# Performance work log

Measured on AMD Instinct MI355X. Metric: run time of the kernel, lower is better.

The kernel has to match this reference:

```python
import jax, jax.numpy as jnp
import numpy as np

DIM = 2048
N_HEADS = 32
N_KV_HEADS = 8
HEAD_DIM = DIM // N_HEADS  # 64
N_REP = N_HEADS // N_KV_HEADS  # 4
ROPE_BASE = 10000.0


def _rope_cos_sin(seq_len, head_dim, dtype):
    inv_freq = 1.0 / (ROPE_BASE ** (jnp.arange(0, head_dim, 2, dtype=jnp.float32) / head_dim))
    freqs = jnp.arange(seq_len, dtype=jnp.float32)[:, None] * inv_freq[None, :]  # [S, hd/2]
    return jnp.cos(freqs).astype(dtype), jnp.sin(freqs).astype(dtype)


def _apply_rope(x, cos, sin):
    # x: [B, S, H, hd]; cos/sin: [S, hd/2]
    x1, x2 = jnp.split(x, 2, axis=-1)
    c = cos[None, :, None, :]
    s = sin[None, :, None, :]
    return jnp.concatenate([x1 * c - x2 * s, x1 * s + x2 * c], axis=-1)


def setup_inputs() -> dict:
    key = jax.random.key(0)
    ks = jax.random.split(key, 5)
    B, S = 2, 2048
    x = jax.random.normal(ks[0], (B, S, DIM), dtype=jnp.float32)
    scale = 1.0 / np.sqrt(DIM)
    wq = jax.random.normal(ks[1], (DIM, DIM), dtype=jnp.float32) * scale
    wk = jax.random.normal(ks[2], (N_KV_HEADS * HEAD_DIM, DIM), dtype=jnp.float32) * scale
    wv = jax.random.normal(ks[3], (N_KV_HEADS * HEAD_DIM, DIM), dtype=jnp.float32) * scale
    wo = jax.random.normal(ks[4], (DIM, DIM), dtype=jnp.float32) * scale
    return {"x": x, "wq": wq, "wk": wk, "wv": wv, "wo": wo}


def reference(x, wq, wk, wv, wo):
    B, S, D = x.shape
    # projections (nn.Linear: y = x @ W.T)
    xq = (x @ wq.T).reshape(B, S, N_HEADS, HEAD_DIM)
    xk = (x @ wk.T).reshape(B, S, N_KV_HEADS, HEAD_DIM)
    xv = (x @ wv.T).reshape(B, S, N_KV_HEADS, HEAD_DIM)

    cos, sin = _rope_cos_sin(S, HEAD_DIM, x.dtype)
    xq = _apply_rope(xq, cos, sin)
    xk = _apply_rope(xk, cos, sin)

    # GQA: repeat kv heads
    keys = jnp.repeat(xk, N_REP, axis=2)    # [B, S, H, hd]
    values = jnp.repeat(xv, N_REP, axis=2)

    scores = jnp.einsum('bqhd,bkhd->bhqk', xq, keys) / np.sqrt(HEAD_DIM)
    causal = jnp.tril(jnp.ones((S, S), dtype=bool))
    scores = jnp.where(causal[None, None, :, :], scores, jnp.finfo(scores.dtype).min)
    probs = jax.nn.softmax(scores, axis=-1)
    out = jnp.einsum('bhqk,bkhd->bqhd', probs, values).reshape(B, S, D)
    return out @ wo.T  # dropout in eval mode == identity
```

## Files before the change

kernel.cpp:

```cpp
#include <hip/hip_runtime.h>

typedef __attribute__((ext_vector_type(8))) short bf16x8;
typedef __attribute__((ext_vector_type(4))) float f32x4;
typedef __attribute__((ext_vector_type(4))) unsigned short u16x4;

#define GPTR(p) (const __attribute__((address_space(1))) void*)(p)
#define LPTR(p) (__attribute__((address_space(3))) void*)(p)

static __device__ __forceinline__ unsigned short f2bf(float f) {
  union { float f; unsigned int u; } x; x.f = f;
  unsigned int u = x.u;
  unsigned int r = (u + 0x7fffu + ((u >> 16) & 1u)) >> 16;
  return (unsigned short)r;
}
static __device__ __forceinline__ float bf2f(unsigned short h) {
  union { unsigned int u; float f; } x; x.u = ((unsigned int)h) << 16;
  return x.f;
}
static __device__ __forceinline__ f32x4 f32x4_zero() {
  f32x4 z = {0.f, 0.f, 0.f, 0.f}; return z;
}
static __device__ __forceinline__ unsigned int cvt_pk_bf16(float lo, float hi) {
  unsigned int r;
  asm("v_cvt_pk_bf16_f32 %0, %1, %2" : "=v"(r) : "v"(lo), "v"(hi));
  return r;
}

__global__ void rope_table_kernel(float* __restrict__ costab, float* __restrict__ sintab) {
  int i = blockIdx.x * blockDim.x + threadIdx.x;
  int s = i >> 5, d = i & 31;
  float invf = exp2f(-(float)d * (13.287712379549449f / 32.0f));
  float a = (float)s * invf;
  costab[i] = cosf(a);
  sintab[i] = sinf(a);
}

__global__ void f32_to_bf16(const float* __restrict__ src, unsigned short* __restrict__ dst, int n4) {
  int stride = gridDim.x * blockDim.x;
  for (int i = blockIdx.x * blockDim.x + threadIdx.x; i < n4; i += stride) {
    float4 v = ((const float4*)src)[i];
    u16x4 o;
    o.x = f2bf(v.x); o.y = f2bf(v.y); o.z = f2bf(v.z); o.w = f2bf(v.w);
    *(u16x4*)(dst + (size_t)i * 4) = o;
  }
}

template<int OUT_BF16>
__global__ __launch_bounds__(256) void gemm_bt(const unsigned short* __restrict__ A,
                                               const unsigned short* __restrict__ B,
                                               void* __restrict__ Cv, int N, int K) {
  __shared__ __align__(16) unsigned short lsA[128 * 32];
  __shared__ __align__(16) unsigned short lsB[128 * 32];
  const int tid = threadIdx.x;
  const int wave = tid >> 6, lane = tid & 63;
  const int fq = lane >> 4, fr = lane & 15;
  const int wr = wave >> 1, wc = wave & 1;
  const int m0 = blockIdx.y * 128, n0 = blockIdx.x * 128;

  const unsigned short* ga0 = A + (size_t)(m0 + (tid >> 2)) * K + ((tid & 3) << 3);
  const unsigned short* ga1 = ga0 + (size_t)64 * K;
  const unsigned short* gb0 = B + (size_t)(n0 + (tid >> 2)) * K + ((tid & 3) << 3);
  const unsigned short* gb1 = gb0 + (size_t)64 * K;
  unsigned short* lA0 = lsA + wave * 512;
  unsigned short* lA1 = lsA + 2048 + wave * 512;
  unsigned short* lB0 = lsB + wave * 512;
  unsigned short* lB1 = lsB + 2048 + wave * 512;

  f32x4 acc[4][4];
#pragma unroll
  for (int i = 0; i < 4; ++i)
#pragma unroll
    for (int j = 0; j < 4; ++j) acc[i][j] = f32x4_zero();

  for (int k0 = 0; k0 < K; k0 += 32) {
    __syncthreads();
    __builtin_amdgcn_global_load_lds(GPTR(ga0 + k0), LPTR(lA0), 16, 0, 0);
    __builtin_amdgcn_global_load_lds(GPTR(ga1 + k0), LPTR(lA1), 16, 0, 0);
    __builtin_amdgcn_global_load_lds(GPTR(gb0 + k0), LPTR(lB0), 16, 0, 0);
    __builtin_amdgcn_global_load_lds(GPTR(gb1 + k0), LPTR(lB1), 16, 0, 0);
    __syncthreads();
    bf16x8 af[4], bfr[4];
#pragma unroll
    for (int f = 0; f < 4; ++f) {
      af[f]  = *(const bf16x8*)(lsA + (wr * 64 + f * 16 + fr) * 32 + fq * 8);
      bfr[f] = *(const bf16x8*)(lsB + (wc * 64 + f * 16 + fr) * 32 + fq * 8);
    }
#pragma unroll
    for (int i = 0; i < 4; ++i)
#pragma unroll
      for (int j = 0; j < 4; ++j)
        acc[i][j] = __builtin_amdgcn_mfma_f32_16x16x32_bf16(af[i], bfr[j], acc[i][j], 0, 0, 0);
  }

#pragma unroll
  for (int i = 0; i < 4; ++i) {
    const int row = m0 + wr * 64 + i * 16 + fq * 4;
#pragma unroll
    for (int j = 0; j < 4; ++j) {
      const int col = n0 + wc * 64 + j * 16 + fr;
#pragma unroll
      for (int v = 0; v < 4; ++v) {
        if (OUT_BF16) ((unsigned short*)Cv)[(size_t)(row + v) * N + col] = f2bf(acc[i][j][v]);
        else          ((float*)Cv)[(size_t)(row + v) * N + col] = acc[i][j][v];
      }
    }
  }
}

__global__ void rope_kernel(unsigned short* __restrict__ qkv,
                            const float* __restrict__ costab,
                            const float* __restrict__ sintab) {
  int idx = blockIdx.x * blockDim.x + threadIdx.x;
  if (idx >= 4096 * 1280) return;
  int row = idx / 1280;
  int p = idx - row * 1280;
  int s = row & 2047;
  int col, d; bool isq;
  if (p < 1024) { isq = true;  d = p & 31; col = (p >> 5) * 64 + d; }
  else { isq = false; int pk = p - 1024; d = pk & 31; col = 2048 + (pk >> 5) * 64 + d; }
  float c = costab[s * 32 + d], sn = sintab[s * 32 + d];
  unsigned short* base = qkv + (size_t)row * 3072;
  float x1 = bf2f(base[col]), x2 = bf2f(base[col + 32]);
  float o1 = x1 * c - x2 * sn;
  float o2 = x1 * sn + x2 * c;
  if (isq) { o1 *= 0.18033688011112042f; o2 *= 0.18033688011112042f; }
  base[col] = f2bf(o1);
  base[col + 32] = f2bf(o2);
}

__global__ __launch_bounds__(512, 4) void flash_attn(const unsigned short* __restrict__ qkv,
                                                     unsigned short* __restrict__ out) {
  __shared__ __align__(16) char K_sh[2 * 8192];
  __shared__ __align__(16) char V_sh[2 * 8192];
  __shared__ __align__(16) char P_sh[8 * 4096];

  const int tid = threadIdx.x;
  const int wave = tid >> 6, lane = tid & 63;
  const int fq = lane >> 4, fr = lane & 15;
  const int b = blockIdx.z, h = blockIdx.y;
  const int qt = gridDim.x - 1 - blockIdx.x;
  const int kvh = h >> 2;
  const int q0 = qt * 256;
  const int wq0 = q0 + wave * 32;
  char* Pw = P_sh + wave * 4096;

  bf16x8 qreg[2][2];
#pragma unroll
  for (int qf = 0; qf < 2; ++qf)
#pragma unroll
    for (int kk = 0; kk < 2; ++kk)
      qreg[qf][kk] = *(const bf16x8*)(qkv + (size_t)(b * 2048 + wq0 + qf * 16 + fr) * 3072
                                      + h * 64 + kk * 32 + fq * 8);

  f32x4 o_acc[4][2];
  float m_run[2], l_run[2];
#pragma unroll
  for (int dc = 0; dc < 4; ++dc) { o_acc[dc][0] = f32x4_zero(); o_acc[dc][1] = f32x4_zero(); }
  m_run[0] = m_run[1] = -1e30f;
  l_run[0] = l_run[1] = 0.f;

  const char* kgbase = (const char*)qkv + (size_t)(b * 2048) * 6144 + 4096 + kvh * 128;
  const unsigned short* vgbase = qkv + (size_t)(b * 2048) * 3072 + 2560 + kvh * 64;
  const int nsteps = (q0 + 256) >> 6;

  const int vk2 = (tid >> 3) << 1;
  const int vc0 = (tid & 7) << 3;
  const int kt = tid - 256;

  {
    if (wave < 4) {
      bf16x8 vv0 = *(const bf16x8*)(vgbase + (size_t)vk2 * 3072 + vc0);
      bf16x8 vv1 = *(const bf16x8*)(vgbase + (size_t)(vk2 + 1) * 3072 + vc0);
#pragma unroll
      for (int j = 0; j < 8; ++j) {
        const int d = vc0 + j;
        const int G = ((d & 7) ^ (d >> 3)) & 7;
        unsigned int w = ((unsigned int)(unsigned short)vv0[j]) |
                         (((unsigned int)(unsigned short)vv1[j]) << 16);
        *(unsigned int*)(V_sh + (d << 7) + ((vk2 << 1) ^ (G << 4))) = w;
      }
    } else {
#pragma unroll
      for (int ld = 0; ld < 2; ++ld) {
        const int row = (kt >> 3) + (ld << 5);
        const int cb = ((kt & 7) << 4) ^ ((row & 7) << 4);
        __builtin_amdgcn_global_load_lds(GPTR(kgbase + (size_t)row * 6144 + cb),
                                         LPTR(K_sh + kt * 16 + ld * 4096), 16, 0, 0);
      }
    }
  }
  __syncthreads();

  int buf = 0;
  for (int st = 0; st < nsteps; ++st) {
    const int k0 = st << 6;
    const bool has_next = (st + 1) < nsteps;
    bf16x8 vv0, vv1;
    if (has_next) {
      const int k0n = k0 + 64;
      if (wave < 4) {
        vv0 = *(const bf16x8*)(vgbase + (size_t)(k0n + vk2) * 3072 + vc0);
        vv1 = *(const bf16x8*)(vgbase + (size_t)(k0n + vk2 + 1) * 3072 + vc0);
      } else {
        char* Kn = K_sh + (buf ^ 1) * 8192;
#pragma unroll
        for (int ld = 0; ld < 2; ++ld) {
          const int row = (kt >> 3) + (ld << 5);
          const int cb = ((kt & 7) << 4) ^ ((row & 7) << 4);
          __builtin_amdgcn_global_load_lds(GPTR(kgbase + (size_t)(k0n + row) * 6144 + cb),
                                           LPTR(Kn + kt * 16 + ld * 4096), 16, 0, 0);
        }
      }
    }

    if (k0 <= wq0 + 31) {
      const char* Kb = K_sh + buf * 8192;
      const char* Vb = V_sh + buf * 8192;
      f32x4 s[2][4];
#pragma unroll
      for (int qf = 0; qf < 2; ++qf)
#pragma unroll
        for (int kf = 0; kf < 4; ++kf) s[qf][kf] = f32x4_zero();
#pragma unroll
      for (int kf = 0; kf < 4; ++kf) {
        const int krow = kf * 16 + fr;
        const int swz = (krow & 7) << 4;
        bf16x8 ka = *(const bf16x8*)(Kb + krow * 128 + ((fq * 16) ^ swz));
        bf16x8 kb = *(const bf16x8*)(Kb + krow * 128 + ((64 + fq * 16) ^ swz));
#pragma unroll
        for (int qf = 0; qf < 2; ++qf) {
          s[qf][kf] = __builtin_amdgcn_mfma_f32_16x16x32_bf16(ka, qreg[qf][0], s[qf][kf], 0, 0, 0);
          s[qf][kf] = __builtin_amdgcn_mfma_f32_16x16x32_bf16(kb, qreg[qf][1], s[qf][kf], 0, 0, 0);
        }
      }
      if (k0 + 63 > wq0) {
#pragma unroll
        for (int qf = 0; qf < 2; ++qf) {
          const int q = wq0 + qf * 16 + fr;
#pragma unroll
          for (int kf = 0; kf < 4; ++kf)
#pragma unroll
            for (int v = 0; v < 4; ++v) {
              const int key = k0 + kf * 16 + fq * 4 + v;
              if (key > q) s[qf][kf][v] = -1e30f;
            }
        }
      }
#pragma unroll
      for (int qf = 0; qf < 2; ++qf) {
        float t = s[qf][0][0];
#pragma unroll
        for (int kf = 0; kf < 4; ++kf)
#pragma unroll
          for (int v = 0; v < 4; ++v) t = fmaxf(t, s[qf][kf][v]);
        t = fmaxf(t, __shfl_xor(t, 16));
        t = fmaxf(t, __shfl_xor(t, 32));
        const float mo = m_run[qf];
        const float mn = fmaxf(mo, t);
        const float sc = __builtin_amdgcn_exp2f(mo - mn);
        m_run[qf] = mn;
        float ps = 0.f;
#pragma unroll
        for (int kf = 0; kf < 4; ++kf)
#pragma unroll
          for (int v = 0; v < 4; ++v) {
            const float p = __builtin_amdgcn_exp2f(s[qf][kf][v] - mn);
            s[qf][kf][v] = p;
            ps += p;
          }
        ps += __shfl_xor(ps, 16);
        ps += __shfl_xor(ps, 32);
        l_run[qf] = l_run[qf] * sc + ps;
#pragma unroll
        for (int dc = 0; dc < 4; ++dc) o_acc[dc][qf] *= sc;
        const int r = qf * 16 + fr;
        const int rswz = (r & 7) << 4;
#pragma unroll
        for (int kf = 0; kf < 4; ++kf) {
          uint2 w;
          w.x = cvt_pk_bf16(s[qf][kf][0], s[qf][kf][1]);
          w.y = cvt_pk_bf16(s[qf][kf][2], s[qf][kf][3]);
          *(uint2*)(Pw + r * 128 + ((kf * 32 + fq * 8) ^ rswz)) = w;
        }
      }
      asm volatile("s_waitcnt lgkmcnt(0)" ::: "memory");
      __builtin_amdgcn_sched_barrier(0);
      const int fswz = (fr & 7) << 4;
#pragma unroll
      for (int kk = 0; kk < 2; ++kk) {
        bf16x8 pa0 = *(const bf16x8*)(Pw + fr * 128 + ((kk * 64 + fq * 16) ^ fswz));
        bf16x8 pa1 = *(const bf16x8*)(Pw + (16 + fr) * 128 + ((kk * 64 + fq * 16) ^ fswz));
#pragma unroll
        for (int dc = 0; dc < 4; ++dc) {
          const int d = dc * 16 + fr;
          const int G = ((d & 7) ^ (d >> 3)) & 7;
          bf16x8 vt = *(const bf16x8*)(Vb + d * 128 + ((kk * 64 + fq * 16) ^ (G << 4)));
          o_acc[dc][0] = __builtin_amdgcn_mfma_f32_16x16x32_bf16(vt, pa0, o_acc[dc][0], 0, 0, 0);
          o_acc[dc][1] = __builtin_amdgcn_mfma_f32_16x16x32_bf16(vt, pa1, o_acc[dc][1], 0, 0, 0);
        }
      }
    }

    if (has_next && wave < 4) {
      char* Vn = V_sh + (buf ^ 1) * 8192;
#pragma unroll
      for (int j = 0; j < 8; ++j) {
        const int d = vc0 + j;
        const int G = ((d & 7) ^ (d >> 3)) & 7;
        unsigned int w = ((unsigned int)(unsigned short)vv0[j]) |
                         (((unsigned int)(unsigned short)vv1[j]) << 16);
        *(unsigned int*)(Vn + (d << 7) + ((vk2 << 1) ^ (G << 4))) = w;
      }
    }
    __syncthreads();
    buf ^= 1;
  }

#pragma unroll
  for (int qf = 0; qf < 2; ++qf) {
    const float inv = 1.0f / l_run[qf];
    const size_t row = (size_t)(b * 2048 + wq0 + qf * 16 + fr);
#pragma unroll
    for (int dc = 0; dc < 4; ++dc) {
      u16x4 o;
#pragma unroll
      for (int v = 0; v < 4; ++v) o[v] = f2bf(o_acc[dc][qf][v] * inv);
      *(u16x4*)(out + row * 2048 + h * 64 + dc * 16 + fq * 4) = o;
    }
  }
}

extern "C" void kernel_launch(void* const* d_in, const int* in_sizes, int n_in,
                              void* d_out, int out_size, void* d_ws, size_t ws_size,
                              hipStream_t stream) {
  (void)in_sizes; (void)n_in; (void)out_size; (void)ws_size;
  const float* x  = (const float*)d_in[0];
  const float* wq = (const float*)d_in[1];
  const float* wk = (const float*)d_in[2];
  const float* wv = (const float*)d_in[3];
  const float* wo = (const float*)d_in[4];

  char* wsb = (char*)d_ws;
  unsigned short* xb     = (unsigned short*)(wsb);
  unsigned short* attn_o = xb;
  unsigned short* wqkvb  = (unsigned short*)(wsb + 16777216);
  unsigned short* wob    = (unsigned short*)(wsb + 29360128);
  unsigned short* qkv    = (unsigned short*)(wsb + 37748736);
  float* costab          = (float*)(wsb + 62914560);
  float* sintab          = (float*)(wsb + 63176704);

  rope_table_kernel<<<256, 256, 0, stream>>>(costab, sintab);

  f32_to_bf16<<<2048, 256, 0, stream>>>(x,  xb,                 8388608 / 4);
  f32_to_bf16<<<1024, 256, 0, stream>>>(wq, wqkvb,              4194304 / 4);
  f32_to_bf16<<<256,  256, 0, stream>>>(wk, wqkvb + 4194304,    1048576 / 4);
  f32_to_bf16<<<256,  256, 0, stream>>>(wv, wqkvb + 5242880,    1048576 / 4);
  f32_to_bf16<<<1024, 256, 0, stream>>>(wo, wob,                4194304 / 4);

  gemm_bt<1><<<dim3(24, 32), 256, 0, stream>>>(xb, wqkvb, (void*)qkv, 3072, 2048);

  rope_kernel<<<20480, 256, 0, stream>>>(qkv, costab, sintab);

  flash_attn<<<dim3(8, 32, 2), 512, 0, stream>>>(qkv, attn_o);

  gemm_bt<0><<<dim3(16, 32), 256, 0, stream>>>(attn_o, wob, d_out, 2048, 2048);
}
```

Baseline: 276.8 us.

## Replace GEMM with double-buffered 8-wave 256x256 kernel using swizzled LDS

Replaces the simple 128x128 single-buffer GEMM with a 512-thread kernel that uses 256-wide tiles, BK=64 and double-buffered LDS. Global-to-LDS loads for the next k-tile are spread across four MFMA phases so they overlap compute. The LDS layout is XOR-swizzled to avoid bank conflicts, and the block index is remapped across XCDs for better L2 locality. It also raises wave priority during MFMA bursts. In exchange it uses much more LDS and registers, so occupancy may drop, and the grid is small (192/256 blocks), which risks load imbalance across CUs.

After: 260.1 us. 6.0% less time.

```diff
diff --git a/kernel.cpp b/kernel.cpp
--- a/kernel.cpp
+++ b/kernel.cpp
@@ -45,56 +45,130 @@
   }
 }
 
-template<int OUT_BF16>
-__global__ __launch_bounds__(256) void gemm_bt(const unsigned short* __restrict__ A,
-                                               const unsigned short* __restrict__ B,
-                                               void* __restrict__ Cv, int N, int K) {
-  __shared__ __align__(16) unsigned short lsA[128 * 32];
-  __shared__ __align__(16) unsigned short lsB[128 * 32];
+template<int FM, int OUT_BF16>
+__global__ __launch_bounds__(512, 2) void gemm8p(const unsigned short* __restrict__ A,
+                                                 const unsigned short* __restrict__ B,
+                                                 void* __restrict__ Cv,
+                                                 int M, int N, int K, int nbx) {
+  constexpr int BM = FM * 32;
+  constexpr int MH = FM / 2;
+  constexpr int ABYTES = BM * 128;
+  constexpr int BBYTES = 256 * 128;
+  __shared__ __align__(16) char lds_all[2 * ABYTES + 2 * BBYTES];
+  char* lsA = lds_all;
+  char* lsB = lds_all + 2 * ABYTES;
+
   const int tid = threadIdx.x;
   const int wave = tid >> 6, lane = tid & 63;
   const int fq = lane >> 4, fr = lane & 15;
-  const int wr = wave >> 1, wc = wave & 1;
-  const int m0 = blockIdx.y * 128, n0 = blockIdx.x * 128;
-
-  const unsigned short* ga0 = A + (size_t)(m0 + (tid >> 2)) * K + ((tid & 3) << 3);
-  const unsigned short* ga1 = ga0 + (size_t)64 * K;
-  const unsigned short* gb0 = B + (size_t)(n0 + (tid >> 2)) * K + ((tid & 3) << 3);
-  const unsigned short* gb1 = gb0 + (size_t)64 * K;
-  unsigned short* lA0 = lsA + wave * 512;
-  unsigned short* lA1 = lsA + 2048 + wave * 512;
-  unsigned short* lB0 = lsB + wave * 512;
-  unsigned short* lB1 = lsB + 2048 + wave * 512;
-
-  f32x4 acc[4][4];
-#pragma unroll
-  for (int i = 0; i < 4; ++i)
+  const int wr = wave >> 2, wc = wave & 3;
+
+  const int nwg = gridDim.x;
+  const int q8 = nwg >> 3;
+  const int sw = (blockIdx.x & 7) * q8 + (blockIdx.x >> 3);
+  const int by = sw / nbx;
+  const int bx = sw - by * nbx;
+  const int m0 = by * BM, n0 = bx * 256;
+
+  const int arow = tid >> 3;
+  const int scol = (((tid & 7) ^ (arow & 7)) << 4);
+
+#define STAGE_A(bufv, kt, h)                                                                  \
+  do {                                                                                        \
+    const char* src_ = (const char*)A + ((size_t)(m0 + (h) * 128 + arow) * K + (kt) * 64) * 2 + scol; \
+    char* dst_ = lsA + (bufv) * ABYTES + (h) * 16384 + tid * 16;                              \
+    __builtin_amdgcn_global_load_lds(GPTR(src_), LPTR(dst_), 16, 0, 0);                       \
+    __builtin_amdgcn_global_load_lds(GPTR(src_ + (size_t)64 * K * 2), LPTR(dst_ + 8192), 16, 0, 0); \
+  } while (0)
+#define STAGE_B(bufv, kt, h)                                                                  \
+  do {                                                                                        \
+    const char* src_ = (const char*)B + ((size_t)(n0 + (h) * 128 + arow) * K + (kt) * 64) * 2 + scol; \
+    char* dst_ = lsB + (bufv) * BBYTES + (h) * 16384 + tid * 16;                              \
+    __builtin_amdgcn_global_load_lds(GPTR(src_), LPTR(dst_), 16, 0, 0);                       \
+    __builtin_amdgcn_global_load_lds(GPTR(src_ + (size_t)64 * K * 2), LPTR(dst_ + 8192), 16, 0, 0); \
+  } while (0)
+
+  f32x4 acc[FM][4];
+#pragma unroll
+  for (int i = 0; i < FM; ++i)
 #pragma unroll
     for (int j = 0; j < 4; ++j) acc[i][j] = f32x4_zero();
 
-  for (int k0 = 0; k0 < K; k0 += 32) {
-    __syncthreads();
-    __builtin_amdgcn_global_load_lds(GPTR(ga0 + k0), LPTR(lA0), 16, 0, 0);
-    __builtin_amdgcn_global_load_lds(GPTR(ga1 + k0), LPTR(lA1), 16, 0, 0);
-    __builtin_amdgcn_global_load_lds(GPTR(gb0 + k0), LPTR(lB0), 16, 0, 0);
-    __builtin_amdgcn_global_load_lds(GPTR(gb1 + k0), LPTR(lB1), 16, 0, 0);
-    __syncthreads();
-    bf16x8 af[4], bfr[4];
-#pragma unroll
-    for (int f = 0; f < 4; ++f) {
-      af[f]  = *(const bf16x8*)(lsA + (wr * 64 + f * 16 + fr) * 32 + fq * 8);
-      bfr[f] = *(const bf16x8*)(lsB + (wc * 64 + f * 16 + fr) * 32 + fq * 8);
-    }
-#pragma unroll
-    for (int i = 0; i < 4; ++i)
-#pragma unroll
-      for (int j = 0; j < 4; ++j)
-        acc[i][j] = __builtin_amdgcn_mfma_f32_16x16x32_bf16(af[i], bfr[j], acc[i][j], 0, 0, 0);
-  }
-
-#pragma unroll
-  for (int i = 0; i < 4; ++i) {
-    const int row = m0 + wr * 64 + i * 16 + fq * 4;
+#define PHASE(p)                                                                              \
+  do {                                                                                        \
+    constexpr int mh = (p) >> 1, nh = (p) & 1;                                                \
+    bf16x8 af[MH][2], bfv[2][2];                                                              \
+    _Pragma("unroll") for (int m = 0; m < MH; ++m) {                                          \
+      const int rowA = wr * FM * 16 + mh * MH * 16 + m * 16 + fr;                             \
+      const char* pa = lsA + buf * ABYTES + (rowA >> 7) * 16384 + (rowA & 127) * 128;         \
+      const int sz = (rowA & 7) << 4;                                                         \
+      af[m][0] = *(const bf16x8*)(pa + ((fq * 16) ^ sz));                                     \
+      af[m][1] = *(const bf16x8*)(pa + ((64 + fq * 16) ^ sz));                                \
+    }                                                                                         \
+    _Pragma("unroll") for (int n = 0; n < 2; ++n) {                                           \
+      const int rowB = wc * 64 + nh * 32 + n * 16 + fr;                                       \
+      const char* pb = lsB + buf * BBYTES + (rowB >> 7) * 16384 + (rowB & 127) * 128;         \
+      const int sz = (rowB & 7) << 4;                                                         \
+      bfv[n][0] = *(const bf16x8*)(pb + ((fq * 16) ^ sz));                                    \
+      bfv[n][1] = *(const bf16x8*)(pb + ((64 + fq * 16) ^ sz));                               \
+    }                                                                                         \
+    asm volatile("s_waitcnt lgkmcnt(0)" ::: "memory");                                        \
+    __builtin_amdgcn_sched_barrier(0);                                                        \
+    __builtin_amdgcn_s_setprio(1);                                                            \
+    _Pragma("unroll") for (int m = 0; m < MH; ++m)                                            \
+      _Pragma("unroll") for (int n = 0; n < 2; ++n) {                                         \
+        acc[mh * MH + m][nh * 2 + n] =                                                        \
+            __builtin_amdgcn_mfma_f32_16x16x32_bf16(af[m][0], bfv[n][0], acc[mh * MH + m][nh * 2 + n], 0, 0, 0); \
+        acc[mh * MH + m][nh * 2 + n] =                                                        \
+            __builtin_amdgcn_mfma_f32_16x16x32_bf16(af[m][1], bfv[n][1], acc[mh * MH + m][nh * 2 + n], 0, 0, 0); \
+      }                                                                                       \
+    __builtin_amdgcn_s_setprio(0);                                                            \
+  } while (0)
+
+  const int NT = K >> 6;
+
+  STAGE_A(0, 0, 0);
+  if constexpr (FM == 8) STAGE_A(0, 0, 1);
+  STAGE_B(0, 0, 0);
+  STAGE_B(0, 0, 1);
+  asm volatile("s_waitcnt vmcnt(0)" ::: "memory");
+  __builtin_amdgcn_s_barrier();
+
+  int buf = 0;
+  for (int t = 0; t < NT; ++t) {
+    const bool hn = (t + 1) < NT;
+    if (hn) {
+      STAGE_A(buf ^ 1, t + 1, 0);
+      asm volatile("s_waitcnt vmcnt(2)" ::: "memory");
+    } else {
+      asm volatile("s_waitcnt vmcnt(0)" ::: "memory");
+    }
+    __builtin_amdgcn_s_barrier();
+    PHASE(0);
+    __builtin_amdgcn_s_barrier();
+    if (hn) {
+      if constexpr (FM == 8) STAGE_A(buf ^ 1, t + 1, 1);
+      else                   STAGE_B(buf ^ 1, t + 1, 0);
+    }
+    PHASE(1);
+    __builtin_amdgcn_s_barrier();
+    if (hn) {
+      if constexpr (FM == 8) STAGE_B(buf ^ 1, t + 1, 0);
+      else                   STAGE_B(buf ^ 1, t + 1, 1);
+    }
+    PHASE(2);
+    __builtin_amdgcn_s_barrier();
+    if (hn) {
+      if constexpr (FM == 8) STAGE_B(buf ^ 1, t + 1, 1);
+    }
+    PHASE(3);
+    __builtin_amdgcn_s_barrier();
+    buf ^= 1;
+  }
+
+#pragma unroll
+  for (int i = 0; i < FM; ++i) {
+    const int row = m0 + wr * FM * 16 + i * 16 + fq * 4;
 #pragma unroll
     for (int j = 0; j < 4; ++j) {
       const int col = n0 + wc * 64 + j * 16 + fr;
@@ -105,6 +179,9 @@
       }
     }
   }
+#undef STAGE_A
+#undef STAGE_B
+#undef PHASE
 }
 
 __global__ void rope_kernel(unsigned short* __restrict__ qkv,
@@ -357,11 +434,11 @@
   f32_to_bf16<<<256,  256, 0, stream>>>(wv, wqkvb + 5242880,    1048576 / 4);
   f32_to_bf16<<<1024, 256, 0, stream>>>(wo, wob,                4194304 / 4);
 
-  gemm_bt<1><<<dim3(24, 32), 256, 0, stream>>>(xb, wqkvb, (void*)qkv, 3072, 2048);
+  gemm8p<8, 1><<<192, 512, 0, stream>>>(xb, wqkvb, (void*)qkv, 4096, 3072, 2048, 12);
 
   rope_kernel<<<20480, 256, 0, stream>>>(qkv, costab, sintab);
 
   flash_attn<<<dim3(8, 32, 2), 512, 0, stream>>>(qkv, attn_o);
 
-  gemm_bt<0><<<dim3(16, 32), 256, 0, stream>>>(attn_o, wob, d_out, 2048, 2048);
-}
+  gemm8p<4, 0><<<256, 512, 0, stream>>>(attn_o, wob, d_out, 4096, 2048, 2048, 8);
+}
```
